# Kernel tuning notes

Hardware: AMD Instinct MI355X
Metric: run time of the kernel (lower is better)

## Reference

```python
import jax, jax.numpy as jnp
import numpy as np

# ---- static skeleton structure (SMPL 24-joint, 23-edge kinematic tree) ----
SMPL_EDGES = [[0,1],[0,2],[0,3],[1,4],[2,5],[3,6],[4,7],[5,8],[6,9],[7,10],
              [8,11],[9,12],[9,13],[9,14],[12,15],[13,16],[14,17],[16,18],
              [17,19],[18,20],[19,21],[20,22],[21,23]]
KERNEL, STRIDE, PAD, DIST = 15, 2, 7, 1

def _edge_dist(edges):
    E = len(edges)
    m = np.full((E, E), 1e6)
    np.fill_diagonal(m, 0.0)
    for i, a in enumerate(edges):
        for j, b in enumerate(edges):
            if i != j and set(a) & set(b):
                m[i, j] = 1.0
    for k in range(E):  # Floyd-Warshall on the edge adjacency graph
        m = np.minimum(m, m[:, k:k+1] + m[k:k+1, :])
    return m

def _find_neighbor(edges, d, n_global):
    m = _edge_dist(edges); E = len(edges)
    nb = [list(np.nonzero(m[i] <= d)[0]) for i in range(E)]
    gp = list(nb[0])  # edges near root edge (keeps deep-motion-editing's known quirk)
    g_ids = [E + k for k in range(n_global)]
    for i in gp:
        nb[i].extend(g_ids)
    for _ in range(n_global):
        nb.append(gp + g_ids)
    return nb

def _find_seqs(edges):
    deg = {}
    for a, b in edges:
        deg[a] = deg.get(a, 0) + 1
        deg[b] = deg.get(b, 0) + 1
    seqs = []
    def rec(j, seq):
        if deg.get(j, 0) > 2 and j != 0:
            seqs.append(seq); seq = []
        if deg.get(j, 0) == 1:
            seqs.append(seq); return
        for idx, (a, b) in enumerate(edges):
            if a == j:
                rec(b, seq + [idx])
    rec(0, [])
    return seqs

def _pooling(edges, last_pool, global_ids):
    pools, new_edges = [], []
    for seq in _find_seqs(edges):
        if last_pool:
            pools.append(seq); continue
        if len(seq) % 2 == 1:
            pools.append([seq[0]]); new_edges.append(edges[seq[0]]); seq = seq[1:]
        for i in range(0, len(seq), 2):
            pools.append([seq[i], seq[i+1]])
            new_edges.append([edges[seq[i]][0], edges[seq[i+1]][1]])
    pools.append(list(global_ids))
    return pools, new_edges

def _conv_mask(nb, in_per, out_per):
    N = len(nb)
    mask = np.zeros((N*out_per, N*in_per, 1), np.float32)
    for i, ns in enumerate(nb):
        for j in ns:
            mask[i*out_per:(i+1)*out_per, j*in_per:(j+1)*in_per, 0] = 1.0
    return mask

def _pool_matrix(pools, n_nodes, cpe):
    W = np.zeros((len(pools)*cpe, n_nodes*cpe), np.float32)
    c = np.arange(cpe)
    for i, grp in enumerate(pools):
        for j in grp:
            W[i*cpe + c, j*cpe + c] = 1.0 / len(grp)
    return W

E0 = len(SMPL_EDGES)
N0 = E0 + 2  # 23 edges + global position node + root-velocity node (the '+4' channels)
MASK0 = jnp.asarray(_conv_mask(_find_neighbor(SMPL_EDGES, DIST, 2), 4, 8))  # (200,100,1)
_pools0, EDGES1 = _pooling(SMPL_EDGES, False, [E0, E0 + 1])
P0 = jnp.asarray(_pool_matrix(_pools0, N0, 8))  # (112,200)
N1 = len(EDGES1) + 1
MASK1 = jnp.asarray(_conv_mask(_find_neighbor(EDGES1, DIST, 1), 8, 16))  # (224,112,1)
_pools1, _ = _pooling(EDGES1, True, [N1 - 1])
P1 = jnp.asarray(_pool_matrix(_pools1, N1, 16))  # (112,224)

IN0, OUT0 = 4 * N0, 8 * N0    # 100, 200
IN1, OUT1 = 8 * N1, 16 * N1   # 112, 224
B, T_IN = 64, 2047            # 2048 frames after zero-frame append


def _skel_conv(x, w, b, mask):
    # masked Conv1d (skeleton-sparse weights), stride 2, zero padding 7, k=15
    y = jax.lax.conv_general_dilated(x, w * mask, window_strides=(STRIDE,),
                                     padding=[(PAD, PAD)],
                                     dimension_numbers=('NCH', 'OIH', 'NCH'))
    return y + b[None, :, None]


def _forward(x, w0, b0, w1, b1):
    # x: (B, T, C); append one zero frame on time dim, then to (B, C, T+1)
    out = jnp.concatenate([x, jnp.zeros_like(x[:, :1, :])], axis=1)
    out = out.transpose(0, 2, 1)
    out = jax.nn.relu(jnp.einsum('pc,bct->bpt', P0, _skel_conv(out, w0, b0, MASK0)))
    out = jax.nn.relu(jnp.einsum('pc,bct->bpt', P1, _skel_conv(out, w1, b1, MASK1)))
    return out  # (B, 112, (T+1)//4)


def setup_inputs() -> dict:
    key = jax.random.key(0)
    k = jax.random.split(key, 5)
    s = 0.05
    return {
        'x':  jax.random.normal(k[0], (B, T_IN, IN0), jnp.float32),
        'w0': jax.random.normal(k[1], (OUT0, IN0, KERNEL), jnp.float32) * s,
        'b0': jax.random.normal(k[2], (OUT0,), jnp.float32) * s,
        'w1': jax.random.normal(k[3], (OUT1, IN1, KERNEL), jnp.float32) * s,
        'b1': jax.random.normal(k[4], (OUT1,), jnp.float32) * s,
    }


def reference(x, w0, b0, w1, b1):
    return _forward(x, w0, b0, w1, b1)
```

## Files before the change

### kernel.cpp

```cpp
#include <hip/hip_runtime.h>


#define OFF_A2  107520u
#define OFF_BF0 322560u
#define OFF_BF1 323008u

typedef unsigned int uint32;
typedef __attribute__((ext_vector_type(8))) short bs8;
typedef __attribute__((ext_vector_type(4))) float f32x4;
union U8 { uint4 u; bs8 s; };

__constant__ int c_pool0_len[14] = {2,2,2,2,1,2,2,1,2,2,1,2,2,2};
__constant__ int c_pool0_mem[14][2] = {{0,3},{6,9},{1,4},{7,10},{2,2},{5,8},{11,14},{12,12},
                                       {15,17},{19,21},{13,13},{16,18},{20,22},{23,24}};
__constant__ unsigned c_nbm0[25] = {
 0x180000Fu,0x1800017u,0x1800027u,0x1800049u,0x92u,0x124u,0x248u,0x490u,
 0x3920u,0x240u,0x480u,0x7900u,0xB900u,0x13900u,0x4800u,0x29000u,
 0x52000u,0xA8000u,0x150000u,0x2A0000u,0x540000u,0x280000u,0x500000u,
 0x180000Fu,0x180000Fu
};
__constant__ int c_pool1_len[7] = {2,2,2,1,3,3,1};
__constant__ int c_pool1_mem[7][3] = {{0,1,1},{2,3,3},{4,5,5},{6,6,6},{7,8,9},{10,11,12},{13,13,13}};
__constant__ unsigned c_nbm1[14] = {
 0x2017u,0x2003u,0x201Du,0xCu,0x2035u,0x4F0u,0x4E0u,0x5E0u,
 0x380u,0x300u,0xCE0u,0x1C00u,0x1800u,0x2017u
};
__constant__ int c_g1p[7][2] = {{0,13},{1,3},{2,4},{5,6},{7,10},{8,11},{9,12}};
__constant__ int c_U1[7][8] = {
 {0,1,2,3,6,23,24,25},
 {3,4,6,7,9,10,25,25},
 {0,1,2,4,5,7,23,24},
 {2,5,8,11,12,13,14,25},
 {8,11,12,13,15,16,25,25},
 {12,13,15,16,17,18,19,20},
 {17,18,19,20,21,22,25,25}};
__constant__ int c_U2[7][8] = {
 {0,1,2,4,13,14,14,14},
 {0,2,3,4,13,14,14,14},
 {0,2,4,5,6,7,10,13},
 {5,6,7,10,14,14,14,14},
 {5,6,7,8,9,10,14,14},
 {5,6,7,10,11,12,14,14},
 {0,1,2,4,13,14,14,14}};
__constant__ unsigned c_pk1a[7] = {0xC0301000u,0xC8483018u,0xB8281000u,0x70604010u,
                                   0xC8786040u,0x98887860u,0xC8A89888u};
__constant__ unsigned c_pk1b[7] = {0xC8B81808u,0xC8503820u,0xC0382008u,0xC8685828u,
                                   0xC8806858u,0xA0908068u,0xC8B0A090u};
__constant__ unsigned c_pk2[7][2] = {
 {0x40201000u,0xE0E0E0D0u},{0x40302000u,0xE0E0E0D0u},{0x50402000u,0xD0A07060u},
 {0xA0706050u,0xE0E0E0E0u},{0x80706050u,0xE0E0A090u},{0xA0706050u,0xE0E0C0B0u},
 {0x40201000u,0xE0E0E0D0u}};

__device__ __forceinline__ uint32 f2bf(float v) {
  uint32 u = __float_as_uint(v);
  return (u + 0x7fffu + ((u >> 16) & 1u)) >> 16;
}

__global__ void prep_fused_weights(const float* __restrict__ w0, const float* __restrict__ b0,
                                   const float* __restrict__ w1, const float* __restrict__ b1,
                                   char* __restrict__ wsb) {
  int t = blockIdx.x * blockDim.x + threadIdx.x;
  if (t < 6720) {
    int lane = t & 63;
    int r = t >> 6;
    int k = r % 15, g = r / 15;
    int m = lane & 15, h = lane >> 4;
    int pool = (m < 8) ? c_g1p[g][0] : c_g1p[g][1];
    int c = m & 7;
    int L = c_pool0_len[pool];
    float inv = 1.f / (float)L;
    uint32 us[8];
#pragma unroll
    for (int j = 0; j < 8; ++j) {
      int node = c_U1[g][2 * h + (j >> 2)];
      int ci = j & 3;
      float v = 0.f;
      if (node < 25) {
        for (int jj = 0; jj < L; ++jj) {
          int mem = c_pool0_mem[pool][jj];
          if ((c_nbm0[mem] >> node) & 1u)
            v += w0[(mem * 8 + c) * 1500 + (node * 4 + ci) * 15 + k];
        }
        v *= inv;
      }
      us[j] = f2bf(v);
    }
    uint4 o = make_uint4(us[0] | (us[1] << 16), us[2] | (us[3] << 16),
                         us[4] | (us[5] << 16), us[6] | (us[7] << 16));
    reinterpret_cast<uint4*>(wsb)[t] = o;
  } else if (t < 6720 + 13440) {
    int t2 = t - 6720;
    int lane = t2 & 63;
    int r = t2 >> 6;
    int k = r % 15;
    int r2 = r / 15;
    int ks = r2 & 1, p = r2 >> 1;
    int c = lane & 15, h = lane >> 4;
    int node = c_U2[p][ks * 4 + h];
    int L = c_pool1_len[p];
    float inv = 1.f / (float)L;
    uint32 us[8];
#pragma unroll
    for (int j = 0; j < 8; ++j) {
      float v = 0.f;
      if (node < 14) {
        for (int jj = 0; jj < L; ++jj) {
          int mem = c_pool1_mem[p][jj];
          if ((c_nbm1[mem] >> node) & 1u)
            v += w1[(mem * 16 + c) * 1680 + (node * 8 + j) * 15 + k];
        }
        v *= inv;
      }
      us[j] = f2bf(v);
    }
    uint4 o = make_uint4(us[0] | (us[1] << 16), us[2] | (us[3] << 16),
                         us[4] | (us[5] << 16), us[6] | (us[7] << 16));
    reinterpret_cast<uint4*>(wsb + OFF_A2)[t2] = o;
  } else if (t < 6720 + 13440 + 112) {
    int p = t - (6720 + 13440);
    int i = p >> 3, c = p & 7;
    int L = c_pool0_len[i];
    float v = 0.f;
    for (int jj = 0; jj < L; ++jj) v += b0[c_pool0_mem[i][jj] * 8 + c];
    reinterpret_cast<float*>(wsb + OFF_BF0)[p] = v / (float)L;
  } else if (t < 6720 + 13440 + 224) {
    int p = t - (6720 + 13440 + 112);
    int i = p >> 4, c = p & 15;
    int L = c_pool1_len[i];
    float v = 0.f;
    for (int jj = 0; jj < L; ++jj) v += b1[c_pool1_mem[i][jj] * 16 + c];
    reinterpret_cast<float*>(wsb + OFF_BF1)[p] = v / (float)L;
  }
}

__global__ __launch_bounds__(896, 4) void conv_fused(const float* __restrict__ x,
                                                     const char* __restrict__ wsb,
                                                     float* __restrict__ out) {
  __shared__ __align__(16) unsigned char lds[173 * 256];
  unsigned char* const xs = lds;
  unsigned char* const ys = lds;
  const int tid = threadIdx.x;
  const int lane = tid & 63;
  const int w = tid >> 6;
  const int g = (w < 7) ? w : (w - 7);
  const int half = (w < 7) ? 0 : 1;
  const int m16 = lane & 15, h = lane >> 4;
  const int b = blockIdx.y;
  const int t0 = blockIdx.x << 5;
  const int f0y = 2 * t0 - 7;
  const int g0x = 4 * t0 - 21;

  const float* __restrict__ xb = x + (size_t)b * (2047 * 100);
  float4 rg[5];
#pragma unroll
  for (int i = 0; i < 5; ++i) {
    rg[i] = make_float4(0.f, 0.f, 0.f, 0.f);
    int e = tid + i * 896;
    if (e < 4325) {
      int f = e / 25, q = e - f * 25;
      int gt = g0x + f;
      if ((unsigned)gt < 2047u)
        rg[i] = *reinterpret_cast<const float4*>(xb + gt * 100 + 4 * q);
    }
  }
  for (int e = tid; e < 173; e += 896)
    *reinterpret_cast<uint2*>(xs + e * 256 + (200u ^ (((e >> 1) & 15) << 3))) =
        make_uint2(0u, 0u);
#pragma unroll
  for (int i = 0; i < 5; ++i) {
    int e = tid + i * 896;
    if (e < 4325) {
      int f = e / 25, q = e - f * 25;
      uint2 wv = make_uint2(f2bf(rg[i].x) | (f2bf(rg[i].y) << 16),
                            f2bf(rg[i].z) | (f2bf(rg[i].w) << 16));
      *reinterpret_cast<uint2*>(xs + f * 256 + ((q * 8) ^ (((f >> 1) & 15) << 3))) = wv;
    }
  }
  const uint4* __restrict__ A1p = reinterpret_cast<const uint4*>(wsb) + g * 960 + lane;
  U8 aw[15];
#pragma unroll
  for (int k = 0; k < 15; ++k) aw[k].u = A1p[k * 64];
  const int pa = c_g1p[g][0], pb = c_g1p[g][1];
  const int chbase = (h < 2) ? (pa * 8 + 4 * h) : (pb * 8 + 4 * (h - 2));
  const float4 bv0 = *reinterpret_cast<const float4*>(wsb + OFF_BF0 + chbase * 4);
  __syncthreads();

  const uint32 offA = (c_pk1a[g] >> (8 * h)) & 255u;
  const uint32 offB = (c_pk1b[g] >> (8 * h)) & 255u;
  f32x4 acc1[3];
  acc1[0] = (f32x4)0.f; acc1[1] = (f32x4)0.f; acc1[2] = (f32x4)0.f;
  if (half == 0) {
#pragma unroll
    for (int k = 0; k < 15; ++k) {
      const uint32 sw = (uint32)(((m16 + (k >> 1)) & 15) << 3);
      const uint32 a0 = offA ^ sw, a1o = offB ^ sw;
      const unsigned char* base = xs + (2 * m16 + k) * 256;
#pragma unroll
      for (int nt = 0; nt < 3; ++nt) {
        uint2 lo = *reinterpret_cast<const uint2*>(base + nt * 8192 + a0);
        uint2 hi = *reinterpret_cast<const uint2*>(base + nt * 8192 + a1o);
        U8 bfr; bfr.u = make_uint4(lo.x, lo.y, hi.x, hi.y);
        acc1[nt] = __builtin_amdgcn_mfma_f32_16x16x32_bf16(aw[k].s, bfr.s, acc1[nt], 0, 0, 0);
      }
    }
  } else {
#pragma unroll
    for (int k = 0; k < 15; ++k) {
      const uint32 sw = (uint32)(((m16 + (k >> 1)) & 15) << 3);
      const uint32 a0 = offA ^ sw, a1o = offB ^ sw;
      const unsigned char* base = xs + (2 * m16 + k) * 256 + 3 * 8192;
#pragma unroll
      for (int nt = 0; nt < 2; ++nt) {
        uint2 lo = *reinterpret_cast<const uint2*>(base + nt * 8192 + a0);
        uint2 hi = *reinterpret_cast<const uint2*>(base + nt * 8192 + a1o);
        U8 bfr; bfr.u = make_uint4(lo.x, lo.y, hi.x, hi.y);
        acc1[nt] = __builtin_amdgcn_mfma_f32_16x16x32_bf16(aw[k].s, bfr.s, acc1[nt], 0, 0, 0);
      }
    }
  }

  const uint4* __restrict__ A2p =
      reinterpret_cast<const uint4*>(wsb + OFF_A2) + g * 1920 + lane;
#pragma unroll
  for (int k = 0; k < 15; ++k) aw[k].u = A2p[k * 64];
  const float4 bv1 = *reinterpret_cast<const float4*>(wsb + OFF_BF1 + (g * 16 + 4 * h) * 4);
  __syncthreads();

  const int ntN = (half == 0) ? 3 : 2;
  const int ntB = (half == 0) ? 0 : 3;
#pragma unroll 3
  for (int ntl = 0; ntl < ntN; ++ntl) {
    int row = (ntB + ntl) * 16 + m16;
    int fy = f0y + row;
    float o0 = fmaxf(acc1[ntl][0] + bv0.x, 0.f);
    float o1 = fmaxf(acc1[ntl][1] + bv0.y, 0.f);
    float o2 = fmaxf(acc1[ntl][2] + bv0.z, 0.f);
    float o3 = fmaxf(acc1[ntl][3] + bv0.w, 0.f);
    uint2 wpk = make_uint2(f2bf(o0) | (f2bf(o1) << 16), f2bf(o2) | (f2bf(o3) << 16));
    if ((unsigned)fy >= 1024u) wpk = make_uint2(0u, 0u);
    *reinterpret_cast<uint2*>(ys + row * 256 +
        (((uint32)(chbase * 2)) ^ (((row >> 1) & 7) << 4))) = wpk;
  }
  for (int e = tid; e < 80; e += 896)
    *reinterpret_cast<uint4*>(ys + e * 256 + (224u ^ (((e >> 1) & 7) << 4))) =
        make_uint4(0u, 0u, 0u, 0u);
  __syncthreads();

  f32x4 acc2 = (f32x4)0.f;
  const uint32 htoff = (uint32)(half * 8192);
  {
    const uint32 noff = (c_pk2[g][0] >> (8 * h)) & 255u;
#pragma unroll
    for (int k = 0; k < 15; ++k) {
      const uint32 sw = (uint32)(((m16 + (k >> 1)) & 7) << 4);
      U8 bf;
      bf.u = *reinterpret_cast<const uint4*>(ys + 2 * m16 * 256 + (noff ^ sw)
                                             + k * 256 + htoff);
      acc2 = __builtin_amdgcn_mfma_f32_16x16x32_bf16(aw[k].s, bf.s, acc2, 0, 0, 0);
    }
  }
#pragma unroll
  for (int k = 0; k < 15; ++k) aw[k].u = A2p[(15 + k) * 64];
  {
    const uint32 noff = (c_pk2[g][1] >> (8 * h)) & 255u;
#pragma unroll
    for (int k = 0; k < 15; ++k) {
      const uint32 sw = (uint32)(((m16 + (k >> 1)) & 7) << 4);
      U8 bf;
      bf.u = *reinterpret_cast<const uint4*>(ys + 2 * m16 * 256 + (noff ^ sw)
                                             + k * 256 + htoff);
      acc2 = __builtin_amdgcn_mfma_f32_16x16x32_bf16(aw[k].s, bf.s, acc2, 0, 0, 0);
    }
  }

  {
    size_t obase = ((size_t)b * 112 + g * 16 + 4 * h) * 512 + t0 + half * 16 + m16;
    out[obase]        = fmaxf(acc2[0] + bv1.x, 0.f);
    out[obase + 512]  = fmaxf(acc2[1] + bv1.y, 0.f);
    out[obase + 1024] = fmaxf(acc2[2] + bv1.z, 0.f);
    out[obase + 1536] = fmaxf(acc2[3] + bv1.w, 0.f);
  }
}

extern "C" void kernel_launch(void* const* d_in, const int* in_sizes, int n_in,
                              void* d_out, int out_size, void* d_ws, size_t ws_size,
                              hipStream_t stream) {
  const float* x  = (const float*)d_in[0];
  const float* w0 = (const float*)d_in[1];
  const float* b0 = (const float*)d_in[2];
  const float* w1 = (const float*)d_in[3];
  const float* b1 = (const float*)d_in[4];
  char* wsb = (char*)d_ws;
  float* out = (float*)d_out;

  prep_fused_weights<<<80, 256, 0, stream>>>(w0, b0, w1, b1, wsb);
  conv_fused<<<dim3(16, 64), 896, 0, stream>>>(x, wsb, out);
}
```

Baseline: 61.49 us.

## Double the time tile per block to reuse weights across more output columns

Each block now computes 64 output frames instead of 32, with a larger LDS staging buffer, more x loads per thread, and two accumulators per wave in the second conv. The grid halves to 8x64 blocks. This amortizes the per-block register weight loads and the halo overlap across twice the work. In exchange the kernel uses more registers and LDS per block, and with 512 blocks of 14 waves it gives less parallelism and occupancy on a 256-CU part.

```diff
diff --git a/kernel.cpp b/kernel.cpp
--- a/kernel.cpp
+++ b/kernel.cpp
@@ -133,10 +133,10 @@
   }
 }
 
-__global__ __launch_bounds__(896, 4) void conv_fused(const float* __restrict__ x,
+__global__ __launch_bounds__(896, 7) void conv_fused(const float* __restrict__ x,
                                                      const char* __restrict__ wsb,
                                                      float* __restrict__ out) {
-  __shared__ __align__(16) unsigned char lds[173 * 256];
+  __shared__ __align__(16) unsigned char lds[301 * 256];
   unsigned char* const xs = lds;
   unsigned char* const ys = lds;
   const int tid = threadIdx.x;
@@ -146,30 +146,30 @@
   const int half = (w < 7) ? 0 : 1;
   const int m16 = lane & 15, h = lane >> 4;
   const int b = blockIdx.y;
-  const int t0 = blockIdx.x << 5;
+  const int t0 = blockIdx.x << 6;
   const int f0y = 2 * t0 - 7;
   const int g0x = 4 * t0 - 21;
 
   const float* __restrict__ xb = x + (size_t)b * (2047 * 100);
-  float4 rg[5];
-#pragma unroll
-  for (int i = 0; i < 5; ++i) {
+  float4 rg[9];
+#pragma unroll
+  for (int i = 0; i < 9; ++i) {
     rg[i] = make_float4(0.f, 0.f, 0.f, 0.f);
     int e = tid + i * 896;
-    if (e < 4325) {
+    if (e < 7525) {
       int f = e / 25, q = e - f * 25;
       int gt = g0x + f;
       if ((unsigned)gt < 2047u)
         rg[i] = *reinterpret_cast<const float4*>(xb + gt * 100 + 4 * q);
     }
   }
-  for (int e = tid; e < 173; e += 896)
+  for (int e = tid; e < 301; e += 896)
     *reinterpret_cast<uint2*>(xs + e * 256 + (200u ^ (((e >> 1) & 15) << 3))) =
         make_uint2(0u, 0u);
 #pragma unroll
-  for (int i = 0; i < 5; ++i) {
+  for (int i = 0; i < 9; ++i) {
     int e = tid + i * 896;
-    if (e < 4325) {
+    if (e < 7525) {
       int f = e / 25, q = e - f * 25;
       uint2 wv = make_uint2(f2bf(rg[i].x) | (f2bf(rg[i].y) << 16),
                             f2bf(rg[i].z) | (f2bf(rg[i].w) << 16));
@@ -187,8 +187,9 @@
 
   const uint32 offA = (c_pk1a[g] >> (8 * h)) & 255u;
   const uint32 offB = (c_pk1b[g] >> (8 * h)) & 255u;
-  f32x4 acc1[3];
-  acc1[0] = (f32x4)0.f; acc1[1] = (f32x4)0.f; acc1[2] = (f32x4)0.f;
+  f32x4 acc1[5];
+#pragma unroll
+  for (int q = 0; q < 5; ++q) acc1[q] = (f32x4)0.f;
   if (half == 0) {
 #pragma unroll
     for (int k = 0; k < 15; ++k) {
@@ -196,7 +197,7 @@
       const uint32 a0 = offA ^ sw, a1o = offB ^ sw;
       const unsigned char* base = xs + (2 * m16 + k) * 256;
 #pragma unroll
-      for (int nt = 0; nt < 3; ++nt) {
+      for (int nt = 0; nt < 5; ++nt) {
         uint2 lo = *reinterpret_cast<const uint2*>(base + nt * 8192 + a0);
         uint2 hi = *reinterpret_cast<const uint2*>(base + nt * 8192 + a1o);
         U8 bfr; bfr.u = make_uint4(lo.x, lo.y, hi.x, hi.y);
@@ -208,9 +209,9 @@
     for (int k = 0; k < 15; ++k) {
       const uint32 sw = (uint32)(((m16 + (k >> 1)) & 15) << 3);
       const uint32 a0 = offA ^ sw, a1o = offB ^ sw;
-      const unsigned char* base = xs + (2 * m16 + k) * 256 + 3 * 8192;
-#pragma unroll
-      for (int nt = 0; nt < 2; ++nt) {
+      const unsigned char* base = xs + (2 * m16 + k) * 256 + 5 * 8192;
+#pragma unroll
+      for (int nt = 0; nt < 4; ++nt) {
         uint2 lo = *reinterpret_cast<const uint2*>(base + nt * 8192 + a0);
         uint2 hi = *reinterpret_cast<const uint2*>(base + nt * 8192 + a1o);
         U8 bfr; bfr.u = make_uint4(lo.x, lo.y, hi.x, hi.y);
@@ -226,9 +227,9 @@
   const float4 bv1 = *reinterpret_cast<const float4*>(wsb + OFF_BF1 + (g * 16 + 4 * h) * 4);
   __syncthreads();
 
-  const int ntN = (half == 0) ? 3 : 2;
-  const int ntB = (half == 0) ? 0 : 3;
-#pragma unroll 3
+  const int ntN = (half == 0) ? 5 : 4;
+  const int ntB = half * 5;
+#pragma unroll 5
   for (int ntl = 0; ntl < ntN; ++ntl) {
     int row = (ntB + ntl) * 16 + m16;
     int fy = f0y + row;
@@ -241,22 +242,25 @@
     *reinterpret_cast<uint2*>(ys + row * 256 +
         (((uint32)(chbase * 2)) ^ (((row >> 1) & 7) << 4))) = wpk;
   }
-  for (int e = tid; e < 80; e += 896)
+  for (int e = tid; e < 144; e += 896)
     *reinterpret_cast<uint4*>(ys + e * 256 + (224u ^ (((e >> 1) & 7) << 4))) =
         make_uint4(0u, 0u, 0u, 0u);
   __syncthreads();
 
-  f32x4 acc2 = (f32x4)0.f;
-  const uint32 htoff = (uint32)(half * 8192);
+  f32x4 acc2[2];
+  acc2[0] = (f32x4)0.f; acc2[1] = (f32x4)0.f;
+  const uint32 htoff = (uint32)(half * 2 * 8192);
   {
     const uint32 noff = (c_pk2[g][0] >> (8 * h)) & 255u;
 #pragma unroll
     for (int k = 0; k < 15; ++k) {
       const uint32 sw = (uint32)(((m16 + (k >> 1)) & 7) << 4);
-      U8 bf;
-      bf.u = *reinterpret_cast<const uint4*>(ys + 2 * m16 * 256 + (noff ^ sw)
-                                             + k * 256 + htoff);
-      acc2 = __builtin_amdgcn_mfma_f32_16x16x32_bf16(aw[k].s, bf.s, acc2, 0, 0, 0);
+      const unsigned char* base = ys + (2 * m16 + k) * 256 + (noff ^ sw) + htoff;
+      U8 b0f, b1f;
+      b0f.u = *reinterpret_cast<const uint4*>(base);
+      b1f.u = *reinterpret_cast<const uint4*>(base + 8192);
+      acc2[0] = __builtin_amdgcn_mfma_f32_16x16x32_bf16(aw[k].s, b0f.s, acc2[0], 0, 0, 0);
+      acc2[1] = __builtin_amdgcn_mfma_f32_16x16x32_bf16(aw[k].s, b1f.s, acc2[1], 0, 0, 0);
     }
   }
 #pragma unroll
@@ -266,19 +270,23 @@
 #pragma unroll
     for (int k = 0; k < 15; ++k) {
       const uint32 sw = (uint32)(((m16 + (k >> 1)) & 7) << 4);
-      U8 bf;
-      bf.u = *reinterpret_cast<const uint4*>(ys + 2 * m16 * 256 + (noff ^ sw)
-                                             + k * 256 + htoff);
-      acc2 = __builtin_amdgcn_mfma_f32_16x16x32_bf16(aw[k].s, bf.s, acc2, 0, 0, 0);
-    }
-  }
-
-  {
-    size_t obase = ((size_t)b * 112 + g * 16 + 4 * h) * 512 + t0 + half * 16 + m16;
-    out[obase]        = fmaxf(acc2[0] + bv1.x, 0.f);
-    out[obase + 512]  = fmaxf(acc2[1] + bv1.y, 0.f);
-    out[obase + 1024] = fmaxf(acc2[2] + bv1.z, 0.f);
-    out[obase + 1536] = fmaxf(acc2[3] + bv1.w, 0.f);
+      const unsigned char* base = ys + (2 * m16 + k) * 256 + (noff ^ sw) + htoff;
+      U8 b0f, b1f;
+      b0f.u = *reinterpret_cast<const uint4*>(base);
+      b1f.u = *reinterpret_cast<const uint4*>(base + 8192);
+      acc2[0] = __builtin_amdgcn_mfma_f32_16x16x32_bf16(aw[k].s, b0f.s, acc2[0], 0, 0, 0);
+      acc2[1] = __builtin_amdgcn_mfma_f32_16x16x32_bf16(aw[k].s, b1f.s, acc2[1], 0, 0, 0);
+    }
+  }
+
+#pragma unroll
+  for (int n = 0; n < 2; ++n) {
+    int nt_s2 = half * 2 + n;
+    size_t obase = ((size_t)b * 112 + g * 16 + 4 * h) * 512 + t0 + nt_s2 * 16 + m16;
+    out[obase]        = fmaxf(acc2[n][0] + bv1.x, 0.f);
+    out[obase + 512]  = fmaxf(acc2[n][1] + bv1.y, 0.f);
+    out[obase + 1024] = fmaxf(acc2[n][2] + bv1.z, 0.f);
+    out[obase + 1536] = fmaxf(acc2[n][3] + bv1.w, 0.f);
   }
 }
 
@@ -294,5 +302,5 @@
   float* out = (float*)d_out;
 
   prep_fused_weights<<<80, 256, 0, stream>>>(w0, b0, w1, b1, wsb);
-  conv_fused<<<dim3(16, 64), 896, 0, stream>>>(x, wsb, out);
+  conv_fused<<<dim3(8, 64), 896, 0, stream>>>(x, wsb, out);
 }
```

Result: slower. 91.47 us (+48.7%).
